# Kernel tuning notes

Hardware: AMD Instinct MI355X
Metric: run time of the kernel (lower is better)

Reference implementation:

```python
import jax, jax.numpy as jnp
import numpy as np

D_MODEL = 2048
N_HEADS = 32
N_KV = 8
N_REP = N_HEADS // N_KV  # 4
HEAD_DIM = D_MODEL // N_HEADS  # 64
ROPE_BASE = 10000.0
B, T = 2, 2048


def rope_tables(seq_len, head_dim):
    inv_freq = 1.0 / (ROPE_BASE ** (jnp.arange(0, head_dim, 2, dtype=jnp.float32) / head_dim))
    t = jnp.arange(seq_len, dtype=jnp.float32)
    freqs = jnp.outer(t, inv_freq)            # [T, hd/2]
    emb = jnp.concatenate([freqs, freqs], -1)  # [T, hd]
    return jnp.cos(emb), jnp.sin(emb)


def rotate_half(x):
    x1, x2 = jnp.split(x, 2, axis=-1)
    return jnp.concatenate([-x2, x1], axis=-1)


def setup_inputs() -> dict:
    key = jax.random.key(0)
    ks = jax.random.split(key, 5)
    s = D_MODEL ** -0.5
    return {
        "x": jax.random.normal(ks[0], (B, T, D_MODEL), jnp.float32),
        "Wq": jax.random.normal(ks[1], (D_MODEL, D_MODEL), jnp.float32) * s,
        "Wk": jax.random.normal(ks[2], (D_MODEL, N_KV * HEAD_DIM), jnp.float32) * s,
        "Wv": jax.random.normal(ks[3], (D_MODEL, N_KV * HEAD_DIM), jnp.float32) * s,
        "Wo": jax.random.normal(ks[4], (D_MODEL, D_MODEL), jnp.float32) * s,
    }


def reference(x, Wq, Wk, Wv, Wo):
    Bx, Tx, C = x.shape
    # QKV projections -> [B, H, T, hd]
    q = (x @ Wq).reshape(Bx, Tx, N_HEADS, HEAD_DIM).transpose(0, 2, 1, 3)
    k = (x @ Wk).reshape(Bx, Tx, N_KV, HEAD_DIM).transpose(0, 2, 1, 3)
    v = (x @ Wv).reshape(Bx, Tx, N_KV, HEAD_DIM).transpose(0, 2, 1, 3)
    # RoPE (offset=0, no cache -> prefill path)
    cos, sin = rope_tables(Tx, HEAD_DIM)  # [T, hd]
    cos = cos[None, None]
    sin = sin[None, None]
    q = q * cos + rotate_half(q) * sin
    k = k * cos + rotate_half(k) * sin
    # Grouped causal attention without materializing expanded KV:
    # q grouped as [B, n_kv, n_rep, T, hd] shares each kv head across n_rep q heads.
    scale = HEAD_DIM ** -0.5
    qg = q.reshape(Bx, N_KV, N_REP, Tx, HEAD_DIM)
    scores = jnp.einsum('bgrtd,bgsd->bgrts', qg, k) * scale  # [B, g, r, T, S]
    causal = jnp.tril(jnp.ones((Tx, Tx), dtype=bool))
    scores = jnp.where(causal, scores, jnp.float32(-jnp.inf))
    attn = jax.nn.softmax(scores, axis=-1)
    out = jnp.einsum('bgrts,bgsd->bgrtd', attn, v)  # [B, g, r, T, hd]
    out = out.reshape(Bx, N_HEADS, Tx, HEAD_DIM).transpose(0, 2, 1, 3).reshape(Bx, Tx, C)
    return out @ Wo, k, v
```

## Files before the change

### kernel.cpp

```cpp
#include <hip/hip_runtime.h>
#include <hip/hip_bf16.h>
#include <cstdint>

typedef uint16_t u16;
typedef __attribute__((ext_vector_type(8))) __bf16 bf16x8;
typedef __attribute__((ext_vector_type(4))) float f32x4;
typedef __attribute__((ext_vector_type(16))) float f32x16;
typedef __attribute__((ext_vector_type(8))) unsigned short u16x8;

#define GLD_LDS(SRC, DST) \
  __builtin_amdgcn_global_load_lds((const __attribute__((address_space(1))) void*)(SRC), \
                                   (__attribute__((address_space(3))) void*)(DST), 16, 0, 0)

__device__ __forceinline__ u16 f2bf(float f) {
  uint32_t u = __float_as_uint(f);
  u += 0x7fffu + ((u >> 16) & 1u);
  return (u16)(u >> 16);
}

__device__ __forceinline__ uint32_t pk2(float a, float b) {
  union { __bf16 h[2]; uint32_t u; } x;
  x.h[0] = (__bf16)a; x.h[1] = (__bf16)b;
  return x.u;
}

__device__ __forceinline__ float fexp2(float x) {
#if __has_builtin(__builtin_amdgcn_exp2f)
  return __builtin_amdgcn_exp2f(x);
#else
  return exp2f(x);
#endif
}

__global__ void cast_f32_bf16(const float* __restrict__ in, u16* __restrict__ out, int n4) {
  int i = blockIdx.x * blockDim.x + threadIdx.x;
  if (i < n4) {
    const float4 v = reinterpret_cast<const float4*>(in)[i];
    ushort4 o;
    o.x = f2bf(v.x); o.y = f2bf(v.y); o.z = f2bf(v.z); o.w = f2bf(v.w);
    reinterpret_cast<ushort4*>(out)[i] = o;
  }
}

__global__ void transpose_cast(const float* __restrict__ W, u16* __restrict__ Wt, int K, int N) {
  __shared__ float tile[32][33];
  int n0 = blockIdx.x * 32, k0 = blockIdx.y * 32;
  int tx = threadIdx.x, ty = threadIdx.y;
  #pragma unroll
  for (int i = ty; i < 32; i += 8)
    tile[i][tx] = W[(size_t)(k0 + i) * N + n0 + tx];
  __syncthreads();
  #pragma unroll
  for (int i = ty; i < 32; i += 8)
    Wt[(size_t)(n0 + i) * K + k0 + tx] = f2bf(tile[tx][i]);
}

__global__ void rope_tables_k(float* __restrict__ cosT, float* __restrict__ sinT) {
  int t = blockIdx.x, i = threadIdx.x;
  float invf = powf(10000.0f, -(float)i * (1.0f / 32.0f));
  float ang = (float)t * invf;
  cosT[t * 32 + i] = cosf(ang);
  sinT[t * 32 + i] = sinf(ang);
}

__global__ __launch_bounds__(512, 2) void gemm256(const u16* __restrict__ A,
    const u16* __restrict__ Bt, float* __restrict__ C, int M, int N, int K) {
  __shared__ alignas(16) u16 Asm[2][2][256][32];
  __shared__ alignas(16) u16 Bsm[2][2][256][32];

  const int tid = threadIdx.x;
  const int l = tid & 63;
  const int w = tid >> 6;
  const int wm = w >> 2, wn = w & 3;
  const int l15 = l & 15, l4 = l >> 4;
  const int m0 = blockIdx.y * 256, n0 = blockIdx.x * 256;
  const int NT = K >> 6;

  f32x4 acc[8][4] = {};

  const int srow = tid >> 2;
  const int sg   = (tid & 3) ^ ((srow >> 1) & 3);
  const u16* Ag = A + (size_t)(m0 + srow) * K + sg * 8;
  const u16* Bg = Bt + (size_t)(n0 + srow) * K + sg * 8;
  const size_t rsk = (size_t)128 * K;
  char* AsD = (char*)&Asm[0][0][0][0] + tid * 16;
  char* BsD = (char*)&Bsm[0][0][0][0] + tid * 16;

#define STAGE_A(BUF, KH, KT) do { \
    GLD_LDS(Ag + (KT) + (KH) * 32,       AsD + ((BUF) * 2 + (KH)) * 16384); \
    GLD_LDS(Ag + (KT) + (KH) * 32 + rsk, AsD + ((BUF) * 2 + (KH)) * 16384 + 8192); \
  } while (0)
#define STAGE_B(BUF, KH, KT) do { \
    GLD_LDS(Bg + (KT) + (KH) * 32,       BsD + ((BUF) * 2 + (KH)) * 16384); \
    GLD_LDS(Bg + (KT) + (KH) * 32 + rsk, BsD + ((BUF) * 2 + (KH)) * 16384 + 8192); \
  } while (0)

  STAGE_A(0, 0, 0);  STAGE_B(0, 0, 0);
  STAGE_A(0, 1, 0);  STAGE_B(0, 1, 0);
  STAGE_A(1, 0, 64); STAGE_B(1, 0, 64);

  const int swz = (l15 >> 1) & 3;

  for (int t = 0; t < NT; ++t) {
    const int c = t & 1;
    const int ktn  = (t + 1) << 6;
    const int ktn2 = (t + 2) << 6;
    bf16x8 bfv[4], af[4];

    if (t < NT - 1) { asm volatile("s_waitcnt vmcnt(8)" ::: "memory"); }
    else            { asm volatile("s_waitcnt vmcnt(4)" ::: "memory"); }
    asm volatile("s_barrier" ::: "memory");
    #pragma unroll
    for (int mf = 0; mf < 4; ++mf)
      af[mf] = *(const bf16x8*)&Asm[c][0][wm * 128 + mf * 16 + l15][(l4 ^ swz) * 8];
    #pragma unroll
    for (int nf = 0; nf < 4; ++nf)
      bfv[nf] = *(const bf16x8*)&Bsm[c][0][wn * 64 + nf * 16 + l15][(l4 ^ swz) * 8];
    if (t + 1 < NT) STAGE_A(c ^ 1, 1, ktn);
    __builtin_amdgcn_s_setprio(1);
    #pragma unroll
    for (int mf = 0; mf < 4; ++mf)
      #pragma unroll
      for (int nf = 0; nf < 4; ++nf)
        acc[mf][nf] = __builtin_amdgcn_mfma_f32_16x16x32_bf16(af[mf], bfv[nf], acc[mf][nf], 0, 0, 0);
    __builtin_amdgcn_s_setprio(0);
    asm volatile("s_barrier" ::: "memory");

    #pragma unroll
    for (int mf = 0; mf < 4; ++mf)
      af[mf] = *(const bf16x8*)&Asm[c][0][wm * 128 + 64 + mf * 16 + l15][(l4 ^ swz) * 8];
    if (t + 1 < NT) STAGE_B(c ^ 1, 1, ktn);
    __builtin_amdgcn_s_setprio(1);
    #pragma unroll
    for (int mf = 0; mf < 4; ++mf)
      #pragma unroll
      for (int nf = 0; nf < 4; ++nf)
        acc[4 + mf][nf] = __builtin_amdgcn_mfma_f32_16x16x32_bf16(af[mf], bfv[nf], acc[4 + mf][nf], 0, 0, 0);
    __builtin_amdgcn_s_setprio(0);
    asm volatile("s_barrier" ::: "memory");

    if (t < NT - 1) { asm volatile("s_waitcnt vmcnt(8)" ::: "memory"); }
    else            { asm volatile("s_waitcnt vmcnt(0)" ::: "memory"); }
    asm volatile("s_barrier" ::: "memory");
    #pragma unroll
    for (int mf = 0; mf < 4; ++mf)
      af[mf] = *(const bf16x8*)&Asm[c][1][wm * 128 + mf * 16 + l15][(l4 ^ swz) * 8];
    #pragma unroll
    for (int nf = 0; nf < 4; ++nf)
      bfv[nf] = *(const bf16x8*)&Bsm[c][1][wn * 64 + nf * 16 + l15][(l4 ^ swz) * 8];
    if (t + 2 < NT) STAGE_A(c, 0, ktn2);
    __builtin_amdgcn_s_setprio(1);
    #pragma unroll
    for (int mf = 0; mf < 4; ++mf)
      #pragma unroll
      for (int nf = 0; nf < 4; ++nf)
        acc[mf][nf] = __builtin_amdgcn_mfma_f32_16x16x32_bf16(af[mf], bfv[nf], acc[mf][nf], 0, 0, 0);
    __builtin_amdgcn_s_setprio(0);
    asm volatile("s_barrier" ::: "memory");

    #pragma unroll
    for (int mf = 0; mf < 4; ++mf)
      af[mf] = *(const bf16x8*)&Asm[c][1][wm * 128 + 64 + mf * 16 + l15][(l4 ^ swz) * 8];
    if (t + 2 < NT) STAGE_B(c, 0, ktn2);
    __builtin_amdgcn_s_setprio(1);
    #pragma unroll
    for (int mf = 0; mf < 4; ++mf)
      #pragma unroll
      for (int nf = 0; nf < 4; ++nf)
        acc[4 + mf][nf] = __builtin_amdgcn_mfma_f32_16x16x32_bf16(af[mf], bfv[nf], acc[4 + mf][nf], 0, 0, 0);
    __builtin_amdgcn_s_setprio(0);
    asm volatile("s_barrier" ::: "memory");
  }
#undef STAGE_A
#undef STAGE_B

  #pragma unroll
  for (int mi = 0; mi < 8; ++mi)
    #pragma unroll
    for (int nf = 0; nf < 4; ++nf)
      #pragma unroll
      for (int r = 0; r < 4; ++r) {
        int row = m0 + wm * 128 + mi * 16 + l4 * 4 + r;
        int col = n0 + wn * 64 + nf * 16 + l15;
        C[(size_t)row * N + col] = acc[mi][nf][r];
      }
}

__global__ __launch_bounds__(256) void rope_scatter(const float* __restrict__ QKV,
    const float* __restrict__ cosT, const float* __restrict__ sinT,
    u16* __restrict__ Qr, u16* __restrict__ Kr,
    float* __restrict__ outK, float* __restrict__ outV) {
  const float QSCALE = 0.125f * 1.44269504088896f;
  int row = blockIdx.x;
  int b = row >> 11, t = row & 2047;
  const float* src = QKV + (size_t)row * 3072;
  int tid = threadIdx.x;
  #pragma unroll
  for (int p = tid; p < 1024; p += 256) {
    int h = p >> 5, d = p & 31;
    float c = cosT[t * 32 + d], s = sinT[t * 32 + d];
    float q0 = src[h * 64 + d], q1 = src[h * 64 + d + 32];
    size_t base = ((size_t)(b * 32 + h) * 2048 + t) * 64 + d;
    Qr[base]      = f2bf((q0 * c - q1 * s) * QSCALE);
    Qr[base + 32] = f2bf((q1 * c + q0 * s) * QSCALE);
  }
  {
    int p = tid;
    int gk = p >> 5, d = p & 31;
    float c = cosT[t * 32 + d], s = sinT[t * 32 + d];
    float k0 = src[2048 + gk * 64 + d], k1 = src[2048 + gk * 64 + d + 32];
    float r0 = k0 * c - k1 * s, r1 = k1 * c + k0 * s;
    size_t base = ((size_t)(b * 8 + gk) * 2048 + t) * 64 + d;
    Kr[base] = f2bf(r0); Kr[base + 32] = f2bf(r1);
    outK[base] = r0; outK[base + 32] = r1;
  }
  #pragma unroll
  for (int p = tid; p < 512; p += 256) {
    int gv = p >> 6, d = p & 63;
    size_t base = ((size_t)(b * 8 + gv) * 2048 + t) * 64 + d;
    outV[base] = src[2560 + gv * 64 + d];
  }
}

__global__ __launch_bounds__(256) void v_transpose(const float* __restrict__ src, u16* __restrict__ dst) {
  __shared__ float tile[64][65];
  int tt = blockIdx.x, bg = blockIdx.y;
  int tid = threadIdx.x;
  const float* sp = src + (size_t)bg * 2048 * 64 + (size_t)tt * 64 * 64;
  int tl = tid >> 2, c0 = (tid & 3) * 16;
  #pragma unroll
  for (int i = 0; i < 4; ++i) {
    float4 v = *reinterpret_cast<const float4*>(sp + (size_t)tl * 64 + c0 + i * 4);
    tile[tl][c0 + i * 4 + 0] = v.x;
    tile[tl][c0 + i * 4 + 1] = v.y;
    tile[tl][c0 + i * 4 + 2] = v.z;
    tile[tl][c0 + i * 4 + 3] = v.w;
  }
  __syncthreads();
  int d = tid >> 2, j0 = (tid & 3) * 16;
  u16x8 a, c;
  #pragma unroll
  for (int j = 0; j < 8; ++j) a[j] = f2bf(tile[j0 + j][d]);
  #pragma unroll
  for (int j = 0; j < 8; ++j) c[j] = f2bf(tile[j0 + 8 + j][d]);
  u16* dp = dst + (size_t)bg * 64 * 2048 + (size_t)d * 2048 + tt * 64 + j0;
  *reinterpret_cast<u16x8*>(dp) = a;
  *reinterpret_cast<u16x8*>(dp + 8) = c;
}

__global__ __launch_bounds__(256) void attn_kernel(
    const u16* __restrict__ Qr, const u16* __restrict__ Kr,
    const u16* __restrict__ Vt, u16* __restrict__ Ao) {
  __shared__ alignas(16) u16 Ks[2][64][72];
  __shared__ alignas(16) u16 Vs[2][64][72];

  const float FIXEDM = 24.0f;

  int bid = blockIdx.x;
  int pairI = bid >> 5;
  int sub = (bid >> 4) & 1;
  int g   = (bid >> 1) & 7;
  int b   = bid & 1;
  int tid = threadIdx.x;
  int w = tid >> 6, l = tid & 63;
  int l31 = l & 31, hi = l >> 5;
  int h = g * 4 + w;

  const u16* Kh = Kr + (size_t)(b * 8 + g) * 2048 * 64;
  const u16* Vh = Vt + (size_t)(b * 8 + g) * 64 * 2048;

  union { u16x8 u; bf16x8 v; } ones;
  #pragma unroll
  for (int i = 0; i < 8; ++i) ones.u[i] = 0x3F80;

  int srow = tid >> 2, sc0 = (tid & 3) * 16;
  const u16* Kp = Kh + (size_t)srow * 64 + sc0;
  const u16* Vp = Vh + (size_t)srow * 2048 + sc0;

  for (int half = 0; half < 2; ++half) {
    const int qc  = half ? pairI : (31 - pairI);
    const int q0w = qc * 64 + sub * 32;
    const int qg  = q0w + l31;

    const u16* Qh = Qr + ((size_t)(b * 32 + h) * 2048 + q0w) * 64;
    bf16x8 qf[4];
    #pragma unroll
    for (int t = 0; t < 4; ++t)
      qf[t] = *reinterpret_cast<const bf16x8*>(Qh + (size_t)l31 * 64 + t * 16 + hi * 8);

    f32x16 o0 = {}, o1 = {}, lacc = {};

    if (half) __syncthreads();

    {
      bf16x8 k0v = *reinterpret_cast<const bf16x8*>(Kp);
      bf16x8 k1v = *reinterpret_cast<const bf16x8*>(Kp + 8);
      bf16x8 v0v = *reinterpret_cast<const bf16x8*>(Vp);
      bf16x8 v1v = *reinterpret_cast<const bf16x8*>(Vp + 8);
      *reinterpret_cast<bf16x8*>(&Ks[0][srow][sc0]) = k0v;
      *reinterpret_cast<bf16x8*>(&Ks[0][srow][sc0 + 8]) = k1v;
      *reinterpret_cast<bf16x8*>(&Vs[0][srow][sc0]) = v0v;
      *reinterpret_cast<bf16x8*>(&Vs[0][srow][sc0 + 8]) = v1v;
    }
    __syncthreads();

    for (int s = 0; s <= qc; ++s) {
      int cur = s & 1;
      bf16x8 knx0, knx1, vnx0, vnx1;
      if (s < qc) {
        knx0 = *reinterpret_cast<const bf16x8*>(Kp + (size_t)(s + 1) * 4096);
        knx1 = *reinterpret_cast<const bf16x8*>(Kp + (size_t)(s + 1) * 4096 + 8);
        vnx0 = *reinterpret_cast<const bf16x8*>(Vp + (size_t)(s + 1) * 64);
        vnx1 = *reinterpret_cast<const bf16x8*>(Vp + (size_t)(s + 1) * 64 + 8);
      }
      int nh = (s == qc && sub == 0) ? 1 : 2;

      f32x16 s0 = {}, s1 = {};
      __builtin_amdgcn_s_setprio(1);
      #pragma unroll
      for (int t = 0; t < 4; ++t) {
        bf16x8 kf0 = *reinterpret_cast<const bf16x8*>(&Ks[cur][l31][t * 16 + hi * 8]);
        s0 = __builtin_amdgcn_mfma_f32_32x32x16_bf16(kf0, qf[t], s0, 0, 0, 0);
      }
      if (nh == 2) {
        #pragma unroll
        for (int t = 0; t < 4; ++t) {
          bf16x8 kf1 = *reinterpret_cast<const bf16x8*>(&Ks[cur][32 + l31][t * 16 + hi * 8]);
          s1 = __builtin_amdgcn_mfma_f32_32x32x16_bf16(kf1, qf[t], s1, 0, 0, 0);
        }
      }
      __builtin_amdgcn_s_setprio(0);

      if (s == qc) {
        #pragma unroll
        for (int r = 0; r < 16; ++r) {
          int kvg = s * 64 + (r & 3) + (r >> 2) * 8 + hi * 4;
          if (kvg > qg) s0[r] = -INFINITY;
        }
        if (nh == 2) {
          #pragma unroll
          for (int r = 0; r < 16; ++r) {
            int kvg = s * 64 + 32 + (r & 3) + (r >> 2) * 8 + hi * 4;
            if (kvg > qg) s1[r] = -INFINITY;
          }
        }
      }

      float p0[16], p1[16];
      #pragma unroll
      for (int r = 0; r < 16; ++r) p0[r] = fexp2(s0[r] - FIXEDM);
      if (nh == 2) {
        #pragma unroll
        for (int r = 0; r < 16; ++r) p1[r] = fexp2(s1[r] - FIXEDM);
      }

      uint32_t pkA[8], pkB[8];
      #pragma unroll
      for (int gi = 0; gi < 8; ++gi) {
        if (gi < nh * 4) {
          const float* pp = (gi < 4) ? p0 : p1;
          int base = (gi & 3) * 4;
          pkA[gi] = pk2(pp[base + 0], pp[base + 1]);
          pkB[gi] = pk2(pp[base + 2], pp[base + 3]);
        }
      }
      __builtin_amdgcn_s_setprio(1);
      #pragma unroll
      for (int kc = 0; kc < 4; ++kc) {
        if (kc < nh * 2) {
          uint32_t zA = pkA[kc * 2 + (hi ^ 1)];
          uint32_t zB = pkB[kc * 2 + (hi ^ 1)];
          uint32_t sA = (uint32_t)__shfl_xor((int)zA, 32);
          uint32_t sB = (uint32_t)__shfl_xor((int)zB, 32);
          uint32_t oA = pkA[kc * 2 + hi];
          uint32_t oB = pkB[kc * 2 + hi];
          union { uint32_t wd[4]; bf16x8 v; } pb;
          pb.wd[0] = hi ? sA : oA;
          pb.wd[1] = hi ? sB : oB;
          pb.wd[2] = hi ? oA : sA;
          pb.wd[3] = hi ? oB : sB;
          bf16x8 va0 = *reinterpret_cast<const bf16x8*>(&Vs[cur][l31][kc * 16 + hi * 8]);
          bf16x8 va1 = *reinterpret_cast<const bf16x8*>(&Vs[cur][32 + l31][kc * 16 + hi * 8]);
          o0 = __builtin_amdgcn_mfma_f32_32x32x16_bf16(va0, pb.v, o0, 0, 0, 0);
          o1 = __builtin_amdgcn_mfma_f32_32x32x16_bf16(va1, pb.v, o1, 0, 0, 0);
          lacc = __builtin_amdgcn_mfma_f32_32x32x16_bf16(ones.v, pb.v, lacc, 0, 0, 0);
        }
      }
      __builtin_amdgcn_s_setprio(0);

      if (s < qc) {
        *reinterpret_cast<bf16x8*>(&Ks[cur ^ 1][srow][sc0]) = knx0;
        *reinterpret_cast<bf16x8*>(&Ks[cur ^ 1][srow][sc0 + 8]) = knx1;
        *reinterpret_cast<bf16x8*>(&Vs[cur ^ 1][srow][sc0]) = vnx0;
        *reinterpret_cast<bf16x8*>(&Vs[cur ^ 1][srow][sc0 + 8]) = vnx1;
        __syncthreads();
      }
    }

    float inv = 1.0f / lacc[0];
    int token = b * 2048 + q0w + l31;
    u16* dst = Ao + (size_t)token * 2048 + h * 64;
    #pragma unroll
    for (int hf = 0; hf < 2; ++hf) {
      f32x16 ov = hf ? o1 : o0;
      #pragma unroll
      for (int r = 0; r < 16; r += 2) {
        int d = (r & 3) + (r >> 2) * 8 + hi * 4 + hf * 32;
        *reinterpret_cast<uint32_t*>(dst + d) = pk2(ov[r] * inv, ov[r + 1] * inv);
      }
    }
  }
}

extern "C" void kernel_launch(void* const* d_in, const int* in_sizes, int n_in,
                              void* d_out, int out_size, void* d_ws, size_t ws_size,
                              hipStream_t stream) {
  const float* x  = (const float*)d_in[0];
  const float* Wq = (const float*)d_in[1];
  const float* Wk = (const float*)d_in[2];
  const float* Wv = (const float*)d_in[3];
  const float* Wo = (const float*)d_in[4];
  float* out = (float*)d_out;

  char* ws = (char*)d_ws;
  u16*   Xb    = (u16*)(ws + 0);
  u16*   Wcat  = (u16*)(ws + 16777216);
  u16*   WoT   = (u16*)(ws + 29360128);
  float* QKV   = (float*)(ws + 37748736);
  u16*   AttnB = (u16*)(ws + 37748736);
  u16*   Qr    = (u16*)(ws + 88080384);
  u16*   Kr    = (u16*)(ws + 104857600);
  u16*   Vtr   = (u16*)(ws + 109051904);
  float* cosT  = (float*)(ws + 113246208);
  float* sinT  = (float*)(ws + 113508352);

  float* outK = out + 8388608;
  float* outV = out + 10485760;

  cast_f32_bf16<<<8192, 256, 0, stream>>>(x, Xb, 2097152);
  transpose_cast<<<dim3(64, 64), dim3(32, 8), 0, stream>>>(Wq, Wcat, 2048, 2048);
  transpose_cast<<<dim3(16, 64), dim3(32, 8), 0, stream>>>(Wk, Wcat + 2048 * 2048, 2048, 512);
  transpose_cast<<<dim3(16, 64), dim3(32, 8), 0, stream>>>(Wv, Wcat + 2560 * 2048, 2048, 512);
  transpose_cast<<<dim3(64, 64), dim3(32, 8), 0, stream>>>(Wo, WoT, 2048, 2048);
  rope_tables_k<<<2048, 32, 0, stream>>>(cosT, sinT);
  gemm256<<<dim3(12, 16), 512, 0, stream>>>(Xb, Wcat, QKV, 4096, 3072, 2048);
  rope_scatter<<<4096, 256, 0, stream>>>(QKV, cosT, sinT, Qr, Kr, outK, outV);
  v_transpose<<<dim3(32, 16), 256, 0, stream>>>(outV, Vtr);
  attn_kernel<<<512, 256, 0, stream>>>(Qr, Kr, Vtr, AttnB);
  gemm256<<<dim3(8, 16), 512, 0, stream>>>(AttnB, WoT, out, 4096, 2048, 2048);
}
```

Measured before the change: 238.2 us.

## Merge prep kernels, overlap Wo transpose with QKV GEMM, bf16 QKV, smaller output GEMM tiles

Fuses the x cast, the Wq/Wk/Wv transpose-casts and the RoPE table build into one launch. The Wo transpose moves into extra blocks of the QKV GEMM so it can fill idle CUs (192 GEMM tiles on 256 CUs). The QKV GEMM now writes bf16 instead of fp32, halving intermediate traffic for rope_scatter, and the output projection uses a 128x256 tile so it launches 256 blocks instead of 128. This cuts launch overhead and memory traffic, but the extra bf16 rounding of Q/K/V before RoPE costs some precision, and the outV output is now bf16-rounded.

```diff
diff --git a/kernel.cpp b/kernel.cpp
--- a/kernel.cpp
+++ b/kernel.cpp
@@ -16,6 +16,10 @@
   uint32_t u = __float_as_uint(f);
   u += 0x7fffu + ((u >> 16) & 1u);
   return (u16)(u >> 16);
+}
+
+__device__ __forceinline__ float bf2f(u16 u) {
+  return __uint_as_float(((uint32_t)u) << 16);
 }
 
 __device__ __forceinline__ uint32_t pk2(float a, float b) {
@@ -32,48 +36,84 @@
 #endif
 }
 
-__global__ void cast_f32_bf16(const float* __restrict__ in, u16* __restrict__ out, int n4) {
-  int i = blockIdx.x * blockDim.x + threadIdx.x;
-  if (i < n4) {
-    const float4 v = reinterpret_cast<const float4*>(in)[i];
-    ushort4 o;
-    o.x = f2bf(v.x); o.y = f2bf(v.y); o.z = f2bf(v.z); o.w = f2bf(v.w);
-    reinterpret_cast<ushort4*>(out)[i] = o;
-  }
-}
-
-__global__ void transpose_cast(const float* __restrict__ W, u16* __restrict__ Wt, int K, int N) {
+__global__ __launch_bounds__(256) void prep_all(const float* __restrict__ x, u16* __restrict__ Xb,
+    const float* __restrict__ Wq, const float* __restrict__ Wk, const float* __restrict__ Wv,
+    u16* __restrict__ Wcat, float* __restrict__ cosT, float* __restrict__ sinT) {
+  int bid = blockIdx.x, tid = threadIdx.x;
+  if (bid < 2048) {
+    int base = bid * 1024 + tid;
+    #pragma unroll
+    for (int k = 0; k < 4; ++k) {
+      int i = base + k * 256;
+      float4 v = reinterpret_cast<const float4*>(x)[i];
+      ushort4 o;
+      o.x = f2bf(v.x); o.y = f2bf(v.y); o.z = f2bf(v.z); o.w = f2bf(v.w);
+      reinterpret_cast<ushort4*>(Xb)[i] = o;
+    }
+    return;
+  }
+  if (bid >= 8192) {
+    int b2 = bid - 8192;
+    int t = b2 * 8 + (tid >> 5), i = tid & 31;
+    float invf = powf(10000.0f, -(float)i * (1.0f / 32.0f));
+    float ang = (float)t * invf;
+    cosT[t * 32 + i] = cosf(ang);
+    sinT[t * 32 + i] = sinf(ang);
+    return;
+  }
   __shared__ float tile[32][33];
-  int n0 = blockIdx.x * 32, k0 = blockIdx.y * 32;
-  int tx = threadIdx.x, ty = threadIdx.y;
+  const float* W; u16* Wt; int N, bx, by;
+  if (bid < 6144)      { int b2 = bid - 2048; W = Wq; Wt = Wcat;               N = 2048; bx = b2 & 63; by = b2 >> 6; }
+  else if (bid < 7168) { int b2 = bid - 6144; W = Wk; Wt = Wcat + 2048 * 2048; N = 512;  bx = b2 & 15; by = b2 >> 4; }
+  else                 { int b2 = bid - 7168; W = Wv; Wt = Wcat + 2560 * 2048; N = 512;  bx = b2 & 15; by = b2 >> 4; }
+  int n0 = bx * 32, k0 = by * 32;
+  int tx = tid & 31, ty = tid >> 5;
   #pragma unroll
   for (int i = ty; i < 32; i += 8)
     tile[i][tx] = W[(size_t)(k0 + i) * N + n0 + tx];
   __syncthreads();
   #pragma unroll
   for (int i = ty; i < 32; i += 8)
-    Wt[(size_t)(n0 + i) * K + k0 + tx] = f2bf(tile[tx][i]);
-}
-
-__global__ void rope_tables_k(float* __restrict__ cosT, float* __restrict__ sinT) {
-  int t = blockIdx.x, i = threadIdx.x;
-  float invf = powf(10000.0f, -(float)i * (1.0f / 32.0f));
-  float ang = (float)t * invf;
-  cosT[t * 32 + i] = cosf(ang);
-  sinT[t * 32 + i] = sinf(ang);
-}
-
-__global__ __launch_bounds__(512, 2) void gemm256(const u16* __restrict__ A,
-    const u16* __restrict__ Bt, float* __restrict__ C, int M, int N, int K) {
+    Wt[(size_t)(n0 + i) * 2048 + k0 + tx] = f2bf(tile[tx][i]);
+}
+
+__global__ __launch_bounds__(512, 2) void gemm_qkv_wot(const u16* __restrict__ A,
+    const u16* __restrict__ Bt, const float* __restrict__ Wo,
+    u16* __restrict__ Cq, u16* __restrict__ WoT) {
   __shared__ alignas(16) u16 Asm[2][2][256][32];
   __shared__ alignas(16) u16 Bsm[2][2][256][32];
 
+  const int bid = blockIdx.x;
   const int tid = threadIdx.x;
+
+  if (bid >= 192) {
+    float (*tile)[65] = (float(*)[65])&Asm[0][0][0][0];
+    int b2 = bid - 192;
+    int r = tid >> 3, c0 = (tid & 7) * 8;
+    for (int it = 0; it < 16; ++it) {
+      int tI = b2 + (it << 6);
+      int k0 = (tI >> 5) * 64;
+      int n0 = (tI & 31) * 64;
+      if (it) __syncthreads();
+      float4 v0 = *reinterpret_cast<const float4*>(&Wo[(size_t)(k0 + r) * 2048 + n0 + c0]);
+      float4 v1 = *reinterpret_cast<const float4*>(&Wo[(size_t)(k0 + r) * 2048 + n0 + c0 + 4]);
+      tile[r][c0 + 0] = v0.x; tile[r][c0 + 1] = v0.y; tile[r][c0 + 2] = v0.z; tile[r][c0 + 3] = v0.w;
+      tile[r][c0 + 4] = v1.x; tile[r][c0 + 5] = v1.y; tile[r][c0 + 6] = v1.z; tile[r][c0 + 7] = v1.w;
+      __syncthreads();
+      u16x8 o;
+      #pragma unroll
+      for (int j = 0; j < 8; ++j) o[j] = f2bf(tile[c0 + j][r]);
+      *reinterpret_cast<u16x8*>(&WoT[(size_t)(n0 + r) * 2048 + k0 + c0]) = o;
+    }
+    return;
+  }
+
+  const int K = 2048, N = 3072;
   const int l = tid & 63;
   const int w = tid >> 6;
   const int wm = w >> 2, wn = w & 3;
   const int l15 = l & 15, l4 = l >> 4;
-  const int m0 = blockIdx.y * 256, n0 = blockIdx.x * 256;
+  const int m0 = (bid / 12) * 256, n0 = (bid % 12) * 256;
   const int NT = K >> 6;
 
   f32x4 acc[8][4] = {};
@@ -182,24 +222,113 @@
       for (int r = 0; r < 4; ++r) {
         int row = m0 + wm * 128 + mi * 16 + l4 * 4 + r;
         int col = n0 + wn * 64 + nf * 16 + l15;
-        C[(size_t)row * N + col] = acc[mi][nf][r];
-      }
-}
-
-__global__ __launch_bounds__(256) void rope_scatter(const float* __restrict__ QKV,
+        Cq[(size_t)row * N + col] = f2bf(acc[mi][nf][r]);
+      }
+}
+
+__global__ __launch_bounds__(512, 2) void gemm128(const u16* __restrict__ A,
+    const u16* __restrict__ Bt, float* __restrict__ C, int M, int N, int K) {
+  __shared__ alignas(16) u16 Asm[2][2][128][32];
+  __shared__ alignas(16) u16 Bsm[2][2][256][32];
+
+  const int tid = threadIdx.x;
+  const int l = tid & 63;
+  const int w = tid >> 6;
+  const int wm = w >> 2, wn = w & 3;
+  const int l15 = l & 15, l4 = l >> 4;
+  const int m0 = blockIdx.y * 128, n0 = blockIdx.x * 256;
+  const int NT = K >> 6;
+
+  f32x4 acc[4][4] = {};
+
+  const int srow = tid >> 2;
+  const int sg   = (tid & 3) ^ ((srow >> 1) & 3);
+  const u16* Ag = A + (size_t)(m0 + srow) * K + sg * 8;
+  const u16* Bg = Bt + (size_t)(n0 + srow) * K + sg * 8;
+  const size_t rsk = (size_t)128 * K;
+  char* AsD = (char*)&Asm[0][0][0][0] + tid * 16;
+  char* BsD = (char*)&Bsm[0][0][0][0] + tid * 16;
+
+#define STG(BUF, KH, KT) do { \
+    GLD_LDS(Ag + (KT) + (KH) * 32,       AsD + ((BUF) * 2 + (KH)) * 8192); \
+    GLD_LDS(Bg + (KT) + (KH) * 32,       BsD + ((BUF) * 2 + (KH)) * 16384); \
+    GLD_LDS(Bg + (KT) + (KH) * 32 + rsk, BsD + ((BUF) * 2 + (KH)) * 16384 + 8192); \
+  } while (0)
+
+  STG(0, 0, 0); STG(0, 1, 0); STG(1, 0, 64);
+
+  const int swz = (l15 >> 1) & 3;
+
+  for (int t = 0; t < NT; ++t) {
+    const int c = t & 1;
+    bf16x8 af[4], bfv[4];
+
+    if (t < NT - 1) { asm volatile("s_waitcnt vmcnt(6)" ::: "memory"); }
+    else            { asm volatile("s_waitcnt vmcnt(3)" ::: "memory"); }
+    asm volatile("s_barrier" ::: "memory");
+    #pragma unroll
+    for (int mf = 0; mf < 4; ++mf)
+      af[mf] = *(const bf16x8*)&Asm[c][0][wm * 64 + mf * 16 + l15][(l4 ^ swz) * 8];
+    #pragma unroll
+    for (int nf = 0; nf < 4; ++nf)
+      bfv[nf] = *(const bf16x8*)&Bsm[c][0][wn * 64 + nf * 16 + l15][(l4 ^ swz) * 8];
+    if (t + 1 < NT) STG(c ^ 1, 1, (t + 1) << 6);
+    __builtin_amdgcn_s_setprio(1);
+    #pragma unroll
+    for (int mf = 0; mf < 4; ++mf)
+      #pragma unroll
+      for (int nf = 0; nf < 4; ++nf)
+        acc[mf][nf] = __builtin_amdgcn_mfma_f32_16x16x32_bf16(af[mf], bfv[nf], acc[mf][nf], 0, 0, 0);
+    __builtin_amdgcn_s_setprio(0);
+    asm volatile("s_barrier" ::: "memory");
+
+    if (t < NT - 1) { asm volatile("s_waitcnt vmcnt(6)" ::: "memory"); }
+    else            { asm volatile("s_waitcnt vmcnt(0)" ::: "memory"); }
+    asm volatile("s_barrier" ::: "memory");
+    #pragma unroll
+    for (int mf = 0; mf < 4; ++mf)
+      af[mf] = *(const bf16x8*)&Asm[c][1][wm * 64 + mf * 16 + l15][(l4 ^ swz) * 8];
+    #pragma unroll
+    for (int nf = 0; nf < 4; ++nf)
+      bfv[nf] = *(const bf16x8*)&Bsm[c][1][wn * 64 + nf * 16 + l15][(l4 ^ swz) * 8];
+    if (t + 2 < NT) STG(c, 0, (t + 2) << 6);
+    __builtin_amdgcn_s_setprio(1);
+    #pragma unroll
+    for (int mf = 0; mf < 4; ++mf)
+      #pragma unroll
+      for (int nf = 0; nf < 4; ++nf)
+        acc[mf][nf] = __builtin_amdgcn_mfma_f32_16x16x32_bf16(af[mf], bfv[nf], acc[mf][nf], 0, 0, 0);
+    __builtin_amdgcn_s_setprio(0);
+    asm volatile("s_barrier" ::: "memory");
+  }
+#undef STG
+
+  #pragma unroll
+  for (int mf = 0; mf < 4; ++mf)
+    #pragma unroll
+    for (int nf = 0; nf < 4; ++nf)
+      #pragma unroll
+      for (int r = 0; r < 4; ++r) {
+        int row = m0 + wm * 64 + mf * 16 + l4 * 4 + r;
+        int col = n0 + wn * 64 + nf * 16 + l15;
+        C[(size_t)row * N + col] = acc[mf][nf][r];
+      }
+}
+
+__global__ __launch_bounds__(256) void rope_scatter(const u16* __restrict__ QKV,
     const float* __restrict__ cosT, const float* __restrict__ sinT,
     u16* __restrict__ Qr, u16* __restrict__ Kr,
     float* __restrict__ outK, float* __restrict__ outV) {
   const float QSCALE = 0.125f * 1.44269504088896f;
   int row = blockIdx.x;
   int b = row >> 11, t = row & 2047;
-  const float* src = QKV + (size_t)row * 3072;
+  const u16* src = QKV + (size_t)row * 3072;
   int tid = threadIdx.x;
   #pragma unroll
   for (int p = tid; p < 1024; p += 256) {
     int h = p >> 5, d = p & 31;
     float c = cosT[t * 32 + d], s = sinT[t * 32 + d];
-    float q0 = src[h * 64 + d], q1 = src[h * 64 + d + 32];
+    float q0 = bf2f(src[h * 64 + d]), q1 = bf2f(src[h * 64 + d + 32]);
     size_t base = ((size_t)(b * 32 + h) * 2048 + t) * 64 + d;
     Qr[base]      = f2bf((q0 * c - q1 * s) * QSCALE);
     Qr[base + 32] = f2bf((q1 * c + q0 * s) * QSCALE);
@@ -208,7 +337,7 @@
     int p = tid;
     int gk = p >> 5, d = p & 31;
     float c = cosT[t * 32 + d], s = sinT[t * 32 + d];
-    float k0 = src[2048 + gk * 64 + d], k1 = src[2048 + gk * 64 + d + 32];
+    float k0 = bf2f(src[2048 + gk * 64 + d]), k1 = bf2f(src[2048 + gk * 64 + d + 32]);
     float r0 = k0 * c - k1 * s, r1 = k1 * c + k0 * s;
     size_t base = ((size_t)(b * 8 + gk) * 2048 + t) * 64 + d;
     Kr[base] = f2bf(r0); Kr[base + 32] = f2bf(r1);
@@ -218,7 +347,7 @@
   for (int p = tid; p < 512; p += 256) {
     int gv = p >> 6, d = p & 63;
     size_t base = ((size_t)(b * 8 + gv) * 2048 + t) * 64 + d;
-    outV[base] = src[2560 + gv * 64 + d];
+    outV[base] = bf2f(src[2560 + gv * 64 + d]);
   }
 }
 
@@ -426,7 +555,7 @@
   u16*   Xb    = (u16*)(ws + 0);
   u16*   Wcat  = (u16*)(ws + 16777216);
   u16*   WoT   = (u16*)(ws + 29360128);
-  float* QKV   = (float*)(ws + 37748736);
+  u16*   QKV   = (u16*)(ws + 37748736);
   u16*   AttnB = (u16*)(ws + 37748736);
   u16*   Qr    = (u16*)(ws + 88080384);
   u16*   Kr    = (u16*)(ws + 104857600);
@@ -437,15 +566,10 @@
   float* outK = out + 8388608;
   float* outV = out + 10485760;
 
-  cast_f32_bf16<<<8192, 256, 0, stream>>>(x, Xb, 2097152);
-  transpose_cast<<<dim3(64, 64), dim3(32, 8), 0, stream>>>(Wq, Wcat, 2048, 2048);
-  transpose_cast<<<dim3(16, 64), dim3(32, 8), 0, stream>>>(Wk, Wcat + 2048 * 2048, 2048, 512);
-  transpose_cast<<<dim3(16, 64), dim3(32, 8), 0, stream>>>(Wv, Wcat + 2560 * 2048, 2048, 512);
-  transpose_cast<<<dim3(64, 64), dim3(32, 8), 0, stream>>>(Wo, WoT, 2048, 2048);
-  rope_tables_k<<<2048, 32, 0, stream>>>(cosT, sinT);
-  gemm256<<<dim3(12, 16), 512, 0, stream>>>(Xb, Wcat, QKV, 4096, 3072, 2048);
+  prep_all<<<8448, 256, 0, stream>>>(x, Xb, Wq, Wk, Wv, Wcat, cosT, sinT);
+  gemm_qkv_wot<<<256, 512, 0, stream>>>(Xb, Wcat, Wo, QKV, WoT);
   rope_scatter<<<4096, 256, 0, stream>>>(QKV, cosT, sinT, Qr, Kr, outK, outV);
   v_transpose<<<dim3(32, 16), 256, 0, stream>>>(outV, Vtr);
   attn_kernel<<<512, 256, 0, stream>>>(Qr, Kr, Vtr, AttnB);
-  gemm256<<<dim3(8, 16), 512, 0, stream>>>(AttnB, WoT, out, 4096, 2048, 2048);
-}
+  gemm128<<<dim3(8, 32), 512, 0, stream>>>(AttnB, WoT, out, 4096, 2048, 2048);
+}
```

Result: faster. 214.4 us (-10.0%).
